# Performance work log

Hardware: AMD Instinct MI355X
Metric: run time of the kernel (lower is better)

## Reference

```python
import jax, jax.numpy as jnp
import numpy as np

B, N, IN_C, OUT_C, H, M, E = 1, 20000, 256, 64, 4, 30, 320000
EPS = 1e-6


def _projection_matrix(m, d, seed=0):
    # NodeFormer create_projection_matrix: stacked transposed-QR blocks, rows
    # rescaled by norms of iid gaussian rows (scaling=0).
    rng = np.random.RandomState(seed)
    blocks = []
    nb_full = m // d
    for _ in range(nb_full):
        q, _ = np.linalg.qr(rng.randn(d, d))
        blocks.append(q.T)
    rem = m - nb_full * d
    if rem > 0:
        q, _ = np.linalg.qr(rng.randn(d, d))
        blocks.append(q.T[:rem])
    final = np.vstack(blocks)
    multiplier = np.linalg.norm(rng.randn(m, d), axis=1)
    return jnp.asarray(multiplier[:, None] * final, dtype=jnp.float32)


def _linear(key, out_f, in_f):
    k1, k2 = jax.random.split(key)
    s = 1.0 / np.sqrt(in_f)
    w = jax.random.uniform(k1, (out_f, in_f), jnp.float32, -s, s)
    b = jax.random.uniform(k2, (out_f,), jnp.float32, -s, s)
    return w, b


def setup_inputs() -> dict:
    key = jax.random.key(0)
    ks = jax.random.split(key, 8)
    Wq_w, Wq_b = _linear(ks[3], H * OUT_C, IN_C)
    Wk_w, Wk_b = _linear(ks[4], H * OUT_C, IN_C)
    Wv_w, Wv_b = _linear(ks[5], H * OUT_C, IN_C)
    Wo_w, Wo_b = _linear(ks[6], OUT_C, H * OUT_C)
    return {
        'z': jax.random.normal(ks[0], (B, N, IN_C), jnp.float32),
        'feat': jax.random.normal(ks[1], (B, N, IN_C), jnp.float32),
        'edge_index': jax.random.randint(ks[2], (2, E), 0, N),
        'tau': jnp.asarray(0.25, jnp.float32),
        'Wq_w': Wq_w, 'Wq_b': Wq_b,
        'Wk_w': Wk_w, 'Wk_b': Wk_b,
        'Wv_w': Wv_w, 'Wv_b': Wv_b,
        'Wo_w': Wo_w, 'Wo_b': Wo_b,
        'b_param': jnp.full((1, H), 0.1, jnp.float32),  # rb_order=1, sigmoid init
        'proj': _projection_matrix(M, OUT_C),
    }


def _softmax_kernel(x, proj, is_query):
    # Performer positive softmax kernel feature map. x: [B,N,H,D] -> [B,N,H,M]
    d = x.shape[-1]
    x = x * (float(d) ** -0.25)
    ratio = 1.0 / jnp.sqrt(jnp.asarray(proj.shape[0], x.dtype))
    xd = jnp.einsum('bnhd,md->bnhm', x, proj)
    diag = 0.5 * jnp.sum(x * x, axis=-1, keepdims=True)
    if is_query:
        mx = jnp.max(xd, axis=-1, keepdims=True)
    else:
        mx = jnp.max(jnp.max(xd, axis=-1, keepdims=True), axis=1, keepdims=True)
    return ratio * (jnp.exp(xd - diag - mx) + EPS)


def reference(z, feat, edge_index, tau, Wq_w, Wq_b, Wk_w, Wk_b, Wv_w, Wv_b,
              Wo_w, Wo_b, b_param, proj):
    Bn, Nn = z.shape[0], z.shape[1]
    q = (feat @ Wq_w.T + Wq_b).reshape(Bn, Nn, H, OUT_C)
    k = (feat @ Wk_w.T + Wk_b).reshape(Bn, Nn, H, OUT_C)
    v = (z @ Wv_w.T + Wv_b).reshape(Bn, Nn, H, OUT_C)

    inv = 1.0 / jnp.sqrt(tau)
    qp = _softmax_kernel(q * inv, proj, True)    # [B,N,H,M]
    kp = _softmax_kernel(k * inv, proj, False)   # [B,N,H,M]

    # Linear (kernelized) attention, O(N*H*M*D)
    kvs = jnp.einsum('bnhm,bnhd->bhmd', kp, v)
    num = jnp.einsum('bnhm,bhmd->bnhd', qp, kvs)
    den = jnp.einsum('bnhm,bhm->bnh', qp, jnp.sum(kp, axis=1))[..., None]
    z_next = num / den                            # [B,N,H,D]

    # Relational bias: GCN-style normalized scatter with per-head scalar weight
    row, col = edge_index[0], edge_index[1]
    d_in = jnp.zeros((Nn,), z.dtype).at[col].add(1.0)
    d_out = jnp.zeros((Nn,), z.dtype).at[row].add(1.0)
    edge_w = jnp.nan_to_num(jnp.sqrt(1.0 / d_in[col]) * jnp.sqrt(1.0 / d_out[row]),
                            nan=0.0, posinf=0.0, neginf=0.0)    # [E]
    msgs = v[:, row] * edge_w[None, :, None, None]              # [B,E,H,D]
    agg = jnp.zeros_like(v).at[:, col].add(msgs)                # [B,N,H,D]
    z_next = z_next + jax.nn.sigmoid(b_param[0])[None, None, :, None] * agg

    out = z_next.reshape(Bn, Nn, H * OUT_C) @ Wo_w.T + Wo_b     # [B,N,OUT_C]
    return out
```

## Files before the change

### kernel.cpp

```cpp
#include <hip/hip_runtime.h>

#define NN 20000
#define EE 320000
#define RATIO_F 0.18257418583505536f
#define EPS_F 1e-6f
#define SCALE_D4 0.35355339059327373f
#define NCH 157

typedef _Float16 f16x8 __attribute__((ext_vector_type(8)));
typedef _Float16 f16x4 __attribute__((ext_vector_type(4)));
typedef float f32x4 __attribute__((ext_vector_type(4)));

__device__ __forceinline__ unsigned fenc(float x) {
  unsigned u = __float_as_uint(x);
  return (u & 0x80000000u) ? ~u : (u | 0x80000000u);
}
__device__ __forceinline__ float fdec(unsigned u) {
  return (u & 0x80000000u) ? __uint_as_float(u & 0x7FFFFFFFu) : __uint_as_float(~u);
}
__device__ __forceinline__ void fma4(float* a, float s, float4 b) {
  a[0] = fmaf(s, b.x, a[0]);
  a[1] = fmaf(s, b.y, a[1]);
  a[2] = fmaf(s, b.z, a[2]);
  a[3] = fmaf(s, b.w, a[3]);
}
__device__ __forceinline__ void gload16(const void* g, void* l) {
  __builtin_amdgcn_global_load_lds(
      (const __attribute__((address_space(1))) unsigned int*)g,
      (__attribute__((address_space(3))) unsigned int*)l, 16, 0, 0);
}

__global__ __launch_bounds__(256)
void k0_build(const float* __restrict__ Wq, const float* __restrict__ Wk,
              const float* __restrict__ Wv, const float* __restrict__ bq,
              const float* __restrict__ bk, const float* __restrict__ bv,
              const float* __restrict__ proj, const float* __restrict__ tau,
              _Float16* __restrict__ Wf, float* __restrict__ bbig) {
  const int col = blockIdx.x;
  const int i = threadIdx.x;
  const float s = rsqrtf(tau[0]) * SCALE_D4;
  float val = 0.f, bias = 0.f;
  if (col < 256) {
    val = Wq[col * 256 + i]; bias = bq[col];
  } else if (col < 512) {
    const int c = col - 256;
    val = Wk[c * 256 + i]; bias = bk[c];
  } else if (col < 768) {
    const int c = col - 512;
    val = Wv[c * 256 + i]; bias = bv[c];
  } else {
    const int rr = col - 768;
    const int grp = rr >> 7;
    const int h = (rr >> 5) & 3, m = rr & 31;
    if (m < 30) {
      const float* W = grp ? Wk : Wq;
      const float* bb = grp ? bk : bq;
      float a = 0.f, ba = 0.f;
#pragma unroll 8
      for (int d = 0; d < 64; ++d) {
        const float pr = proj[m * 64 + d];
        a  = fmaf(pr, W[(h * 64 + d) * 256 + i], a);
        ba = fmaf(pr, bb[h * 64 + d], ba);
      }
      val = s * a; bias = s * ba;
    }
  }
  const int kt = i >> 5, gg = (i >> 3) & 3, j = i & 7;
  const int lane = gg * 16 + (col & 15);
  const size_t off = (size_t)((col >> 4) * 8 + kt) * 512 + lane * 8 + j;
  Wf[off] = (_Float16)val;
  if (i == 0) bbig[col] = bias;
}

__global__ __launch_bounds__(256)
void k0b_wo(const float* __restrict__ Wo, _Float16* __restrict__ WoFh,
            _Float16* __restrict__ WoFl) {
  const int col = blockIdx.x;
  const int i = threadIdx.x;
  const float val = Wo[col * 256 + i];
  const int kt = i >> 5, gg = (i >> 3) & 3, j = i & 7;
  const int lane = gg * 16 + (col & 15);
  const size_t off = (size_t)((col >> 4) * 8 + kt) * 512 + lane * 8 + j;
  const _Float16 hb = (_Float16)val;
  WoFh[off] = hb;
  WoFl[off] = (_Float16)(val - (float)hb);
}

__device__ __forceinline__ void cvt_half(const float4* raw, f16x8* Ah, f16x8* Al) {
#pragma unroll
  for (int kt = 0; kt < 4; ++kt) {
    const float ff[8] = {raw[kt*2].x, raw[kt*2].y, raw[kt*2].z, raw[kt*2].w,
                         raw[kt*2+1].x, raw[kt*2+1].y, raw[kt*2+1].z, raw[kt*2+1].w};
    union { _Float16 h[8]; f16x8 v; } hu, lu;
#pragma unroll
    for (int j = 0; j < 8; ++j) {
      const _Float16 hb = (_Float16)ff[j];
      hu.h[j] = hb;
      lu.h[j] = (_Float16)(ff[j] - (float)hb);
    }
    Ah[kt] = hu.v; Al[kt] = lu.v;
  }
}

__device__ __forceinline__ int ct_of(int s, int isv, int h, int y) {
  if (isv) return 32 + (y - 4) * 8 + s;
  if (s < 4)  return h * 4 + s;
  if (s < 8)  return 16 + h * 4 + (s - 4);
  if (s < 10) return 48 + 2 * h + (s - 8);
  return 56 + 2 * h + (s - 10);
}

__global__ __launch_bounds__(512, 4)
void k1_all(const float* __restrict__ feat, const float* __restrict__ zin,
            const _Float16* __restrict__ Wf, const float* __restrict__ bbig,
            const float* __restrict__ tau,
            float* __restrict__ qp, float* __restrict__ kbuf,
            _Float16* __restrict__ vh, unsigned* __restrict__ kmaxU) {
  __shared__ __align__(16) _Float16 blds[12 * 2048];
  const int t = threadIdx.x;
  const int wid = t >> 6, lane = t & 63;
  const int g = lane >> 4, cl = lane & 15;
  const int y = blockIdx.y;
  const int h = y & 3;
  const int rbase = blockIdx.x * 128 + wid * 16;
  int arow = rbase + cl; if (arow > NN - 1) arow = NN - 1;

  if (y < 4) {
    const float* arp = feat + (size_t)arow * 256;
#pragma unroll
    for (int r = 0; r < 6; ++r) {
      const int idx = r * 4096 + t * 8;
      const int s = idx >> 11, wi = idx & 2047;
      gload16(Wf + (size_t)ct_of(s, 0, h, y) * 4096 + wi, &blds[idx]);
    }
    float4 raw[8];
#pragma unroll
    for (int l = 0; l < 4; ++l) {
      raw[l * 2]     = *(const float4*)(arp + l * 32 + g * 8);
      raw[l * 2 + 1] = *(const float4*)(arp + l * 32 + g * 8 + 4);
    }
    f16x8 Ah[4], Al[4];
    cvt_half(raw, Ah, Al);
    __syncthreads();
#pragma unroll
    for (int l = 0; l < 4; ++l) {
      raw[l * 2]     = *(const float4*)(arp + (l + 4) * 32 + g * 8);
      raw[l * 2 + 1] = *(const float4*)(arp + (l + 4) * 32 + g * 8 + 4);
    }
    f32x4 acc[12];
#pragma unroll
    for (int s = 0; s < 12; ++s) acc[s] = (f32x4){0.f, 0.f, 0.f, 0.f};
#pragma unroll
    for (int ktl = 0; ktl < 4; ++ktl) {
#pragma unroll
      for (int s = 0; s < 12; ++s) {
        const f16x8 b = *(const f16x8*)&blds[s * 2048 + ktl * 512 + lane * 8];
        acc[s] = __builtin_amdgcn_mfma_f32_16x16x32_f16(Ah[ktl], b, acc[s], 0, 0, 0);
        acc[s] = __builtin_amdgcn_mfma_f32_16x16x32_f16(Al[ktl], b, acc[s], 0, 0, 0);
      }
    }
    __syncthreads();
#pragma unroll
    for (int r = 0; r < 6; ++r) {
      const int idx = r * 4096 + t * 8;
      const int s = idx >> 11, wi = idx & 2047;
      gload16(Wf + (size_t)ct_of(s, 0, h, y) * 4096 + 2048 + wi, &blds[idx]);
    }
    cvt_half(raw, Ah, Al);
    __syncthreads();
#pragma unroll
    for (int ktl = 0; ktl < 4; ++ktl) {
#pragma unroll
      for (int s = 0; s < 12; ++s) {
        const f16x8 b = *(const f16x8*)&blds[s * 2048 + ktl * 512 + lane * 8];
        acc[s] = __builtin_amdgcn_mfma_f32_16x16x32_f16(Ah[ktl], b, acc[s], 0, 0, 0);
        acc[s] = __builtin_amdgcn_mfma_f32_16x16x32_f16(Al[ktl], b, acc[s], 0, 0, 0);
      }
    }
#pragma unroll
    for (int s = 0; s < 12; ++s) {
      const float bb = bbig[ct_of(s, 0, h, y) * 16 + cl];
#pragma unroll
      for (int j = 0; j < 4; ++j) acc[s][j] += bb;
    }
    const float sc = rsqrtf(tau[0]) * SCALE_D4;
    const float h2 = 0.5f * sc * sc;
    float dsq[4], dsk[4];
#pragma unroll
    for (int j = 0; j < 4; ++j) {
      dsq[j] = acc[0][j] * acc[0][j] + acc[1][j] * acc[1][j] +
               acc[2][j] * acc[2][j] + acc[3][j] * acc[3][j];
      dsk[j] = acc[4][j] * acc[4][j] + acc[5][j] * acc[5][j] +
               acc[6][j] * acc[6][j] + acc[7][j] * acc[7][j];
    }
#pragma unroll
    for (int m = 1; m < 16; m <<= 1) {
#pragma unroll
      for (int j = 0; j < 4; ++j) {
        dsq[j] += __shfl_xor(dsq[j], m);
        dsk[j] += __shfl_xor(dsk[j], m);
      }
    }
    {
#pragma unroll
      for (int j = 0; j < 4; ++j) {
        const float x0 = acc[8][j], x1 = acc[9][j];
        float mv = fmaxf(x0, (cl < 14) ? x1 : -3.4e38f);
#pragma unroll
        for (int m = 1; m < 16; m <<= 1) mv = fmaxf(mv, __shfl_xor(mv, m));
        const float dg = h2 * dsq[j];
        const int r = rbase + 4 * g + j;
        if (r < NN) {
          float* dst = qp + (size_t)r * 120 + h * 30;
          dst[cl] = RATIO_F * (expf(x0 - dg - mv) + EPS_F);
          if (cl < 14) dst[16 + cl] = RATIO_F * (expf(x1 - dg - mv) + EPS_F);
        }
      }
    }
    {
      float wmax = -3.4e38f;
#pragma unroll
      for (int j = 0; j < 4; ++j) {
        const float x0 = acc[10][j], x1 = acc[11][j];
        float mv = fmaxf(x0, (cl < 14) ? x1 : -3.4e38f);
#pragma unroll
        for (int m = 1; m < 16; m <<= 1) mv = fmaxf(mv, __shfl_xor(mv, m));
        wmax = fmaxf(wmax, mv);
        const float dg = h2 * dsk[j];
        const int r = rbase + 4 * g + j;
        if (r < NN) {
          float* dst = kbuf + (size_t)r * 120 + h * 30;
          dst[cl] = x0 - dg;
          if (cl < 14) dst[16 + cl] = x1 - dg;
        }
      }
      wmax = fmaxf(wmax, __shfl_xor(wmax, 16));
      wmax = fmaxf(wmax, __shfl_xor(wmax, 32));
      if (lane == 0) atomicMax(&kmaxU[h], fenc(wmax));
    }
  } else {
    const float* arp = zin + (size_t)arow * 256;
#pragma unroll
    for (int r = 0; r < 4; ++r) {
      const int idx = r * 4096 + t * 8;
      const int s = idx >> 11, wi = idx & 2047;
      gload16(Wf + (size_t)ct_of(s, 1, h, y) * 4096 + wi, &blds[idx]);
    }
    float4 raw[8];
#pragma unroll
    for (int l = 0; l < 4; ++l) {
      raw[l * 2]     = *(const float4*)(arp + l * 32 + g * 8);
      raw[l * 2 + 1] = *(const float4*)(arp + l * 32 + g * 8 + 4);
    }
    f16x8 Ah[4], Al[4];
    cvt_half(raw, Ah, Al);
    __syncthreads();
#pragma unroll
    for (int l = 0; l < 4; ++l) {
      raw[l * 2]     = *(const float4*)(arp + (l + 4) * 32 + g * 8);
      raw[l * 2 + 1] = *(const float4*)(arp + (l + 4) * 32 + g * 8 + 4);
    }
    f32x4 acc[8];
#pragma unroll
    for (int s = 0; s < 8; ++s) acc[s] = (f32x4){0.f, 0.f, 0.f, 0.f};
#pragma unroll
    for (int ktl = 0; ktl < 4; ++ktl) {
#pragma unroll
      for (int s = 0; s < 8; ++s) {
        const f16x8 b = *(const f16x8*)&blds[s * 2048 + ktl * 512 + lane * 8];
        acc[s] = __builtin_amdgcn_mfma_f32_16x16x32_f16(Ah[ktl], b, acc[s], 0, 0, 0);
        acc[s] = __builtin_amdgcn_mfma_f32_16x16x32_f16(Al[ktl], b, acc[s], 0, 0, 0);
      }
    }
    __syncthreads();
#pragma unroll
    for (int r = 0; r < 4; ++r) {
      const int idx = r * 4096 + t * 8;
      const int s = idx >> 11, wi = idx & 2047;
      gload16(Wf + (size_t)ct_of(s, 1, h, y) * 4096 + 2048 + wi, &blds[idx]);
    }
    cvt_half(raw, Ah, Al);
    __syncthreads();
#pragma unroll
    for (int ktl = 0; ktl < 4; ++ktl) {
#pragma unroll
      for (int s = 0; s < 8; ++s) {
        const f16x8 b = *(const f16x8*)&blds[s * 2048 + ktl * 512 + lane * 8];
        acc[s] = __builtin_amdgcn_mfma_f32_16x16x32_f16(Ah[ktl], b, acc[s], 0, 0, 0);
        acc[s] = __builtin_amdgcn_mfma_f32_16x16x32_f16(Al[ktl], b, acc[s], 0, 0, 0);
      }
    }
#pragma unroll
    for (int s = 0; s < 8; ++s) {
      const int ct = ct_of(s, 1, h, y);
      const float bb = bbig[ct * 16 + cl];
      const int colb = (ct - 32) * 16 + cl;
#pragma unroll
      for (int j = 0; j < 4; ++j) {
        const int r = rbase + 4 * g + j;
        if (r < NN) vh[(size_t)r * 256 + colb] = (_Float16)(acc[s][j] + bb);
      }
    }
  }
}

__global__ __launch_bounds__(256)
void k3_kvs(const float* __restrict__ kbr, const _Float16* __restrict__ vh,
            const unsigned* __restrict__ kmaxU, float* __restrict__ partial) {
  __shared__ float kpch[128 * 32];
  __shared__ float vch[128 * 68];
  const int h = blockIdx.y;
  const int n0 = blockIdx.x * 128;
  const int cnt = min(128, NN - n0);
  const int t = threadIdx.x;
  const float mx = fdec(kmaxU[h]);
  const int m = t >> 3, dg = t & 7, d0 = dg * 8;
#pragma unroll
  for (int l = 0; l < 15; ++l) {
    const int flat = l * 256 + t;
    const int nl = flat / 30, mm = flat - nl * 30;
    kpch[nl * 32 + mm] = (nl < cnt)
        ? RATIO_F * (expf(kbr[(size_t)(n0 + nl) * 120 + h * 30 + mm] - mx) + EPS_F)
        : 0.f;
  }
#pragma unroll
  for (int l = 0; l < 8; ++l) {
    const int f4 = l * 256 + t;
    const int nl = f4 >> 4, dd = (f4 & 15) * 4;
    float4 vv = make_float4(0.f, 0.f, 0.f, 0.f);
    if (nl < cnt) {
      f16x4 u = *(const f16x4*)(vh + (size_t)(n0 + nl) * 256 + h * 64 + dd);
      vv = make_float4((float)u[0], (float)u[1], (float)u[2], (float)u[3]);
    }
    *(float4*)&vch[nl * 68 + dd] = vv;
  }
  __syncthreads();
  float acc[8] = {0, 0, 0, 0, 0, 0, 0, 0};
  float asum = 0.f;
  const int ms = (m < 30) ? m : 0;
  for (int nl = 0; nl < cnt; ++nl) {
    const float kv = kpch[nl * 32 + ms];
    const float4 va = *(const float4*)&vch[nl * 68 + d0];
    const float4 vb = *(const float4*)&vch[nl * 68 + d0 + 4];
    fma4(&acc[0], kv, va);
    fma4(&acc[4], kv, vb);
    asum += kv;
  }
  if (m < 30) {
    float* dst = partial + ((size_t)blockIdx.y * NCH + blockIdx.x) * 1952 + m * 64 + d0;
#pragma unroll
    for (int j = 0; j < 8; ++j) dst[j] = acc[j];
    if (dg == 0)
      partial[((size_t)blockIdx.y * NCH + blockIdx.x) * 1952 + 1920 + m] = asum;
  }
}

__global__ __launch_bounds__(256)
void k3b_reduce(const float* __restrict__ partial, float* __restrict__ kvs,
                float* __restrict__ ksum) {
  const int idx = blockIdx.x * 256 + threadIdx.x;
  if (idx >= 4 * 1952) return;
  const int h = idx / 1952, q = idx - h * 1952;
  float s = 0.f;
  for (int c = 0; c < NCH; ++c)
    s += partial[((size_t)h * NCH + c) * 1952 + q];
  if (q < 1920) kvs[h * 1920 + q] = s;
  else if (q < 1950) ksum[h * 30 + (q - 1920)] = s;
}

__global__ __launch_bounds__(256)
void k4_attn(const float* __restrict__ qp, const float* __restrict__ kvs,
             const float* __restrict__ ksum, float* __restrict__ zbuf) {
  __shared__ float kvsl[120 * 68];
  __shared__ float ksl[120];
  __shared__ float qpl[32 * 120];
  const int t = threadIdx.x;
  const int n0 = blockIdx.x * 32;
#pragma unroll
  for (int l = 0; l < 30; ++l) {
    const int f = l * 256 + t;
    const int hm = f >> 6, d = f & 63;
    kvsl[hm * 68 + d] = kvs[f];
  }
  if (t < 120) ksl[t] = ksum[t];
#pragma unroll
  for (int l = 0; l < 15; ++l) {
    const int f = l * 256 + t;
    qpl[f] = qp[(size_t)n0 * 120 + f];
  }
  __syncthreads();
  const int nl = t >> 3, dg = t & 7, d0 = dg * 8;
  const float* qrow = &qpl[nl * 120];
  float den[4] = {0, 0, 0, 0};
  for (int m = 0; m < 30; ++m) {
#pragma unroll
    for (int hh = 0; hh < 4; ++hh) den[hh] = fmaf(qrow[hh * 30 + m], ksl[hh * 30 + m], den[hh]);
  }
  float acc[4][8] = {};
  for (int m = 0; m < 30; ++m) {
#pragma unroll
    for (int hh = 0; hh < 4; ++hh) {
      const float qv = qrow[hh * 30 + m];
      const float* kr = &kvsl[(hh * 30 + m) * 68 + d0];
      const float4 ka = *(const float4*)kr;
      const float4 kb = *(const float4*)(kr + 4);
      fma4(&acc[hh][0], qv, ka);
      fma4(&acc[hh][4], qv, kb);
    }
  }
  const size_t n = n0 + nl;
#pragma unroll
  for (int hh = 0; hh < 4; ++hh) {
    const float inv = 1.0f / den[hh];
    float4 o1 = make_float4(acc[hh][0] * inv, acc[hh][1] * inv, acc[hh][2] * inv, acc[hh][3] * inv);
    float4 o2 = make_float4(acc[hh][4] * inv, acc[hh][5] * inv, acc[hh][6] * inv, acc[hh][7] * inv);
    *(float4*)(zbuf + n * 256 + hh * 64 + d0) = o1;
    *(float4*)(zbuf + n * 256 + hh * 64 + d0 + 4) = o2;
  }
}

__global__ __launch_bounds__(256)
void k5_deg(const int* __restrict__ ei, int* __restrict__ dini, int* __restrict__ douti) {
  const int q = blockIdx.x * 256 + threadIdx.x;
  if (q >= EE / 4) return;
  const int4 r4 = *(const int4*)(ei + q * 4);
  const int4 c4 = *(const int4*)(ei + EE + q * 4);
  atomicAdd(&dini[c4.x], 1); atomicAdd(&dini[c4.y], 1);
  atomicAdd(&dini[c4.z], 1); atomicAdd(&dini[c4.w], 1);
  atomicAdd(&douti[r4.x], 1); atomicAdd(&douti[r4.y], 1);
  atomicAdd(&douti[r4.z], 1); atomicAdd(&douti[r4.w], 1);
}

__global__ __launch_bounds__(1024)
void k6a_scan(const int* __restrict__ cnt, int* __restrict__ off) {
  __shared__ int s[1024];
  const int t = threadIdx.x;
  int4 v[5];
  int sum = 0;
  const int4* p4 = (const int4*)(cnt + t * 20);
#pragma unroll
  for (int i = 0; i < 5; ++i) {
    v[i] = p4[i];
    sum += v[i].x + v[i].y + v[i].z + v[i].w;
  }
  s[t] = sum;
  __syncthreads();
  for (int o = 1; o < 1024; o <<= 1) {
    const int add = (t >= o) ? s[t - o] : 0;
    __syncthreads();
    s[t] += add;
    __syncthreads();
  }
  int run = (t == 0) ? 0 : s[t - 1];
  if (t == 0) off[0] = 0;
  const int base = t * 20;
#pragma unroll
  for (int i = 0; i < 5; ++i) {
    const int vals[4] = {v[i].x, v[i].y, v[i].z, v[i].w};
#pragma unroll
    for (int j = 0; j < 4; ++j) {
      const int idx = base + i * 4 + j;
      if (idx < NN) { run += vals[j]; off[idx + 1] = run; }
    }
  }
}

__global__ __launch_bounds__(256)
void k6b_fill(const int* __restrict__ ei, const int* __restrict__ coff,
              int* __restrict__ cursor, int* __restrict__ crow) {
  const int e = blockIdx.x * 256 + threadIdx.x;
  const int r = ei[e], c = ei[EE + e];
  const int pos = atomicAdd(&cursor[c], 1);
  crow[coff[c] + pos] = r;
}

__global__ __launch_bounds__(256)
void k6c_rw(const int* __restrict__ douti, float* __restrict__ rw) {
  const int n = blockIdx.x * 256 + threadIdx.x;
  if (n < NN) rw[n] = rsqrtf((float)douti[n]);
}

__global__ __launch_bounds__(256)
void k7g_gather(const int* __restrict__ coff, const int* __restrict__ crow,
                const float* __restrict__ rw, const _Float16* __restrict__ vh,
                _Float16* __restrict__ aggh) {
  const int node = blockIdx.x * 4 + (threadIdx.x >> 6);
  const int lane = threadIdx.x & 63;
  const int o0 = coff[node], o1 = coff[node + 1];
  float a0 = 0.f, a1 = 0.f, a2 = 0.f, a3 = 0.f;
  if (o1 > o0) {
    int e = o0;
    for (; e + 8 <= o1; e += 8) {
      int rr[8];
#pragma unroll
      for (int u = 0; u < 8; ++u) rr[u] = crow[e + u];
      float ww[8];
#pragma unroll
      for (int u = 0; u < 8; ++u) ww[u] = rw[rr[u]];
#pragma unroll
      for (int u = 0; u < 8; ++u) {
        const f16x4 vv = *(const f16x4*)(vh + (size_t)rr[u] * 256 + lane * 4);
        a0 = fmaf(ww[u], (float)vv[0], a0);
        a1 = fmaf(ww[u], (float)vv[1], a1);
        a2 = fmaf(ww[u], (float)vv[2], a2);
        a3 = fmaf(ww[u], (float)vv[3], a3);
      }
    }
    for (; e < o1; ++e) {
      const int r = crow[e];
      const float wr = rw[r];
      const f16x4 vv = *(const f16x4*)(vh + (size_t)r * 256 + lane * 4);
      a0 = fmaf(wr, (float)vv[0], a0);
      a1 = fmaf(wr, (float)vv[1], a1);
      a2 = fmaf(wr, (float)vv[2], a2);
      a3 = fmaf(wr, (float)vv[3], a3);
    }
    const float rin = rsqrtf((float)(o1 - o0));
    a0 *= rin; a1 *= rin; a2 *= rin; a3 *= rin;
  }
  f16x4 st;
  st[0] = (_Float16)a0; st[1] = (_Float16)a1;
  st[2] = (_Float16)a2; st[3] = (_Float16)a3;
  *(f16x4*)(aggh + (size_t)node * 256 + lane * 4) = st;
}

__global__ __launch_bounds__(512, 4)
void k8m_out(const float* __restrict__ zbuf, const _Float16* __restrict__ aggh,
             const _Float16* __restrict__ WoFh, const _Float16* __restrict__ WoFl,
             const float* __restrict__ bo, const float* __restrict__ bp,
             float* __restrict__ out) {
  __shared__ __align__(16) _Float16 blds[8 * 4096];
  const int t = threadIdx.x;
  const int wid = t >> 6, lane = t & 63;
  const int g = lane >> 4, cl = lane & 15;
  const int rbase = blockIdx.x * 128 + wid * 16;
  int arow = rbase + cl; if (arow > NN - 1) arow = NN - 1;
#pragma unroll
  for (int s = 0; s < 4; ++s) {
    gload16(WoFh + (size_t)s * 4096 + t * 8, &blds[(s * 512 + t) * 8]);
    gload16(WoFl + (size_t)s * 4096 + t * 8, &blds[((s + 4) * 512 + t) * 8]);
  }
  float sgv[4];
#pragma unroll
  for (int hh = 0; hh < 4; ++hh) sgv[hh] = 1.f / (1.f + expf(-bp[hh]));
  const float* zr = zbuf + (size_t)arow * 256;
  const _Float16* ar = aggh + (size_t)arow * 256;
  f16x8 Ah[8], Al[8];
#pragma unroll
  for (int kt = 0; kt < 8; ++kt) {
    const float4 z0 = *(const float4*)(zr + kt * 32 + g * 8);
    const float4 z1 = *(const float4*)(zr + kt * 32 + g * 8 + 4);
    const f16x4 g0 = *(const f16x4*)(ar + kt * 32 + g * 8);
    const f16x4 g1 = *(const f16x4*)(ar + kt * 32 + g * 8 + 4);
    const float sg = sgv[kt >> 1];
    const float ff[8] = {
        z0.x + sg * (float)g0[0], z0.y + sg * (float)g0[1],
        z0.z + sg * (float)g0[2], z0.w + sg * (float)g0[3],
        z1.x + sg * (float)g1[0], z1.y + sg * (float)g1[1],
        z1.z + sg * (float)g1[2], z1.w + sg * (float)g1[3]};
    union { _Float16 h[8]; f16x8 v; } hu, lu;
#pragma unroll
    for (int j = 0; j < 8; ++j) {
      const _Float16 hb = (_Float16)ff[j];
      hu.h[j] = hb;
      lu.h[j] = (_Float16)(ff[j] - (float)hb);
    }
    Ah[kt] = hu.v; Al[kt] = lu.v;
  }
  __syncthreads();
  f32x4 acc[4];
#pragma unroll
  for (int s = 0; s < 4; ++s) acc[s] = (f32x4){0.f, 0.f, 0.f, 0.f};
#pragma unroll
  for (int kt = 0; kt < 8; ++kt) {
#pragma unroll
    for (int s = 0; s < 4; ++s) {
      const f16x8 bh = *(const f16x8*)&blds[s * 4096 + kt * 512 + lane * 8];
      const f16x8 bl = *(const f16x8*)&blds[(s + 4) * 4096 + kt * 512 + lane * 8];
      acc[s] = __builtin_amdgcn_mfma_f32_16x16x32_f16(Ah[kt], bh, acc[s], 0, 0, 0);
      acc[s] = __builtin_amdgcn_mfma_f32_16x16x32_f16(Ah[kt], bl, acc[s], 0, 0, 0);
      acc[s] = __builtin_amdgcn_mfma_f32_16x16x32_f16(Al[kt], bh, acc[s], 0, 0, 0);
    }
  }
#pragma unroll
  for (int s = 0; s < 4; ++s) {
    const float bb = bo[s * 16 + cl];
#pragma unroll
    for (int j = 0; j < 4; ++j) {
      const int r = rbase + 4 * g + j;
      if (r < NN) out[(size_t)r * 64 + s * 16 + cl] = acc[s][j] + bb;
    }
  }
}

extern "C" void kernel_launch(void* const* d_in, const int* in_sizes, int n_in,
                              void* d_out, int out_size, void* d_ws, size_t ws_size,
                              hipStream_t stream) {
  (void)in_sizes; (void)n_in; (void)out_size; (void)ws_size;
  const float* z    = (const float*)d_in[0];
  const float* feat = (const float*)d_in[1];
  const int*   ei   = (const int*)d_in[2];
  const float* tau  = (const float*)d_in[3];
  const float* Wq_w = (const float*)d_in[4];
  const float* Wq_b = (const float*)d_in[5];
  const float* Wk_w = (const float*)d_in[6];
  const float* Wk_b = (const float*)d_in[7];
  const float* Wv_w = (const float*)d_in[8];
  const float* Wv_b = (const float*)d_in[9];
  const float* Wo_w = (const float*)d_in[10];
  const float* Wo_b = (const float*)d_in[11];
  const float* bp   = (const float*)d_in[12];
  const float* proj = (const float*)d_in[13];
  float* out = (float*)d_out;

  char* p = (char*)d_ws;
  auto alloc = [&](size_t bytes) { char* r = p; p += (bytes + 255) & ~(size_t)255; return r; };
  _Float16* Wf    = (_Float16*)alloc((size_t)256 * 1024 * 2);
  _Float16* WoFh  = (_Float16*)alloc((size_t)64 * 256 * 2);
  _Float16* WoFl  = (_Float16*)alloc((size_t)64 * 256 * 2);
  float*    bbig  = (float*)alloc(1024 * 4);
  _Float16* vh    = (_Float16*)alloc((size_t)NN * 256 * 2);
  _Float16* aggh  = (_Float16*)alloc((size_t)NN * 256 * 2);
  float*    qp    = (float*)alloc((size_t)NN * 120 * 4);
  float*    kbuf  = (float*)alloc((size_t)NN * 120 * 4);
  float*    zbuf  = (float*)alloc((size_t)NN * 256 * 4);
  float*    partial = (float*)alloc((size_t)4 * NCH * 1952 * 4);
  float*    kvs   = (float*)alloc(7680 * 4);
  float*    ksum  = (float*)alloc(120 * 4);
  float*    rw    = (float*)alloc((size_t)NN * 4);
  char* z0 = p;
  unsigned* kmaxU = (unsigned*)alloc(16);
  int*      dini  = (int*)alloc((size_t)20480 * 4);
  int*      douti = (int*)alloc((size_t)NN * 4);
  int*      cursor= (int*)alloc((size_t)NN * 4);
  char* z1 = p;
  int*      coff  = (int*)alloc((size_t)(NN + 1) * 4);
  int*      crow  = (int*)alloc((size_t)EE * 4);

  hipMemsetAsync(z0, 0, (size_t)(z1 - z0), stream);

  k0_build<<<1024, 256, 0, stream>>>(Wq_w, Wk_w, Wv_w, Wq_b, Wk_b, Wv_b, proj, tau, Wf, bbig);
  k0b_wo<<<64, 256, 0, stream>>>(Wo_w, WoFh, WoFl);
  k5_deg<<<(EE / 4 + 255) / 256, 256, 0, stream>>>(ei, dini, douti);
  k6a_scan<<<1, 1024, 0, stream>>>(dini, coff);
  k6b_fill<<<EE / 256, 256, 0, stream>>>(ei, coff, cursor, crow);
  k6c_rw<<<(NN + 255) / 256, 256, 0, stream>>>(douti, rw);
  k1_all<<<dim3(157, 6), 512, 0, stream>>>(feat, z, Wf, bbig, tau, qp, kbuf, vh, kmaxU);
  k7g_gather<<<NN / 4, 256, 0, stream>>>(coff, crow, rw, vh, aggh);
  k3_kvs<<<dim3(NCH, 4), 256, 0, stream>>>(kbuf, vh, kmaxU, partial);
  k3b_reduce<<<(4 * 1952 + 255) / 256, 256, 0, stream>>>(partial, kvs, ksum);
  k4_attn<<<NN / 32, 256, 0, stream>>>(qp, kvs, ksum, zbuf);
  k8m_out<<<157, 512, 0, stream>>>(zbuf, aggh, WoFh, WoFl, Wo_b, bp, out);
}
```

Baseline: 280.5 us.

## Store qp and z in fp16, fuse bias-add into attention, merge small kernels

The query feature map qp and the pre-output activation z are now stored as fp16 instead of fp32, which halves their memory traffic. The sigmoid-weighted relational-bias add moves from the output GEMM into k4_attn. The output GEMM drops the low-part split MFMA for activations, so it runs two MFMAs per tile instead of three. The Wo conversion kernel merges into k0_build and the fill and rw kernels merge into one launch, cutting launch overhead. The cost is reduced precision in the activations feeding the final projection.

Result: faster. 257.2 us (-8.3%).

```diff
diff --git a/kernel.cpp b/kernel.cpp
--- a/kernel.cpp
+++ b/kernel.cpp
@@ -35,9 +35,23 @@
               const float* __restrict__ Wv, const float* __restrict__ bq,
               const float* __restrict__ bk, const float* __restrict__ bv,
               const float* __restrict__ proj, const float* __restrict__ tau,
-              _Float16* __restrict__ Wf, float* __restrict__ bbig) {
-  const int col = blockIdx.x;
+              const float* __restrict__ Wo,
+              _Float16* __restrict__ Wf, float* __restrict__ bbig,
+              _Float16* __restrict__ WoFh, _Float16* __restrict__ WoFl) {
+  const int blk = blockIdx.x;
   const int i = threadIdx.x;
+  const int kt = i >> 5, gg = (i >> 3) & 3, j = i & 7;
+  if (blk >= 1024) {
+    const int col = blk - 1024;
+    const float val = Wo[col * 256 + i];
+    const int lane = gg * 16 + (col & 15);
+    const size_t off = (size_t)((col >> 4) * 8 + kt) * 512 + lane * 8 + j;
+    const _Float16 hb = (_Float16)val;
+    WoFh[off] = hb;
+    WoFl[off] = (_Float16)(val - (float)hb);
+    return;
+  }
+  const int col = blk;
   const float s = rsqrtf(tau[0]) * SCALE_D4;
   float val = 0.f, bias = 0.f;
   if (col < 256) {
@@ -65,25 +79,10 @@
       val = s * a; bias = s * ba;
     }
   }
-  const int kt = i >> 5, gg = (i >> 3) & 3, j = i & 7;
   const int lane = gg * 16 + (col & 15);
   const size_t off = (size_t)((col >> 4) * 8 + kt) * 512 + lane * 8 + j;
   Wf[off] = (_Float16)val;
   if (i == 0) bbig[col] = bias;
-}
-
-__global__ __launch_bounds__(256)
-void k0b_wo(const float* __restrict__ Wo, _Float16* __restrict__ WoFh,
-            _Float16* __restrict__ WoFl) {
-  const int col = blockIdx.x;
-  const int i = threadIdx.x;
-  const float val = Wo[col * 256 + i];
-  const int kt = i >> 5, gg = (i >> 3) & 3, j = i & 7;
-  const int lane = gg * 16 + (col & 15);
-  const size_t off = (size_t)((col >> 4) * 8 + kt) * 512 + lane * 8 + j;
-  const _Float16 hb = (_Float16)val;
-  WoFh[off] = hb;
-  WoFl[off] = (_Float16)(val - (float)hb);
 }
 
 __device__ __forceinline__ void cvt_half(const float4* raw, f16x8* Ah, f16x8* Al) {
@@ -114,7 +113,7 @@
 void k1_all(const float* __restrict__ feat, const float* __restrict__ zin,
             const _Float16* __restrict__ Wf, const float* __restrict__ bbig,
             const float* __restrict__ tau,
-            float* __restrict__ qp, float* __restrict__ kbuf,
+            _Float16* __restrict__ qph, float* __restrict__ kbuf,
             _Float16* __restrict__ vh, unsigned* __restrict__ kmaxU) {
   __shared__ __align__(16) _Float16 blds[12 * 2048];
   const int t = threadIdx.x;
@@ -211,9 +210,10 @@
         const float dg = h2 * dsq[j];
         const int r = rbase + 4 * g + j;
         if (r < NN) {
-          float* dst = qp + (size_t)r * 120 + h * 30;
-          dst[cl] = RATIO_F * (expf(x0 - dg - mv) + EPS_F);
-          if (cl < 14) dst[16 + cl] = RATIO_F * (expf(x1 - dg - mv) + EPS_F);
+          _Float16* dst = qph + (size_t)r * 120 + h * 30;
+          dst[cl] = (_Float16)(RATIO_F * (expf(x0 - dg - mv) + EPS_F));
+          if (cl < 14)
+            dst[16 + cl] = (_Float16)(RATIO_F * (expf(x1 - dg - mv) + EPS_F));
         }
       }
     }
@@ -369,8 +369,9 @@
 }
 
 __global__ __launch_bounds__(256)
-void k4_attn(const float* __restrict__ qp, const float* __restrict__ kvs,
-             const float* __restrict__ ksum, float* __restrict__ zbuf) {
+void k4_attn(const _Float16* __restrict__ qph, const float* __restrict__ kvs,
+             const float* __restrict__ ksum, const _Float16* __restrict__ aggh,
+             const float* __restrict__ bp, _Float16* __restrict__ zh) {
   __shared__ float kvsl[120 * 68];
   __shared__ float ksl[120];
   __shared__ float qpl[32 * 120];
@@ -386,7 +387,7 @@
 #pragma unroll
   for (int l = 0; l < 15; ++l) {
     const int f = l * 256 + t;
-    qpl[f] = qp[(size_t)n0 * 120 + f];
+    qpl[f] = (float)qph[(size_t)n0 * 120 + f];
   }
   __syncthreads();
   const int nl = t >> 3, dg = t & 7, d0 = dg * 8;
@@ -412,10 +413,13 @@
 #pragma unroll
   for (int hh = 0; hh < 4; ++hh) {
     const float inv = 1.0f / den[hh];
-    float4 o1 = make_float4(acc[hh][0] * inv, acc[hh][1] * inv, acc[hh][2] * inv, acc[hh][3] * inv);
-    float4 o2 = make_float4(acc[hh][4] * inv, acc[hh][5] * inv, acc[hh][6] * inv, acc[hh][7] * inv);
-    *(float4*)(zbuf + n * 256 + hh * 64 + d0) = o1;
-    *(float4*)(zbuf + n * 256 + hh * 64 + d0 + 4) = o2;
+    const float sg = 1.f / (1.f + expf(-bp[hh]));
+    const f16x8 ag = *(const f16x8*)(aggh + n * 256 + hh * 64 + d0);
+    f16x8 o;
+#pragma unroll
+    for (int jj = 0; jj < 8; ++jj)
+      o[jj] = (_Float16)(acc[hh][jj] * inv + sg * (float)ag[jj]);
+    *(f16x8*)(zh + n * 256 + hh * 64 + d0) = o;
   }
 }
 
@@ -466,18 +470,19 @@
 }
 
 __global__ __launch_bounds__(256)
-void k6b_fill(const int* __restrict__ ei, const int* __restrict__ coff,
-              int* __restrict__ cursor, int* __restrict__ crow) {
-  const int e = blockIdx.x * 256 + threadIdx.x;
-  const int r = ei[e], c = ei[EE + e];
-  const int pos = atomicAdd(&cursor[c], 1);
-  crow[coff[c] + pos] = r;
-}
-
-__global__ __launch_bounds__(256)
-void k6c_rw(const int* __restrict__ douti, float* __restrict__ rw) {
-  const int n = blockIdx.x * 256 + threadIdx.x;
-  if (n < NN) rw[n] = rsqrtf((float)douti[n]);
+void k6bc(const int* __restrict__ ei, const int* __restrict__ coff,
+          int* __restrict__ cursor, int* __restrict__ crow,
+          const int* __restrict__ douti, float* __restrict__ rw) {
+  const int b = blockIdx.x;
+  if (b < EE / 256) {
+    const int e = b * 256 + threadIdx.x;
+    const int r = ei[e], c = ei[EE + e];
+    const int pos = atomicAdd(&cursor[c], 1);
+    crow[coff[c] + pos] = r;
+  } else {
+    const int n = (b - EE / 256) * 256 + threadIdx.x;
+    if (n < NN) rw[n] = rsqrtf((float)douti[n]);
+  }
 }
 
 __global__ __launch_bounds__(256)
@@ -525,9 +530,8 @@
 }
 
 __global__ __launch_bounds__(512, 4)
-void k8m_out(const float* __restrict__ zbuf, const _Float16* __restrict__ aggh,
-             const _Float16* __restrict__ WoFh, const _Float16* __restrict__ WoFl,
-             const float* __restrict__ bo, const float* __restrict__ bp,
+void k8m_out(const _Float16* __restrict__ zh, const _Float16* __restrict__ WoFh,
+             const _Float16* __restrict__ WoFl, const float* __restrict__ bo,
              float* __restrict__ out) {
   __shared__ __align__(16) _Float16 blds[8 * 4096];
   const int t = threadIdx.x;
@@ -540,33 +544,11 @@
     gload16(WoFh + (size_t)s * 4096 + t * 8, &blds[(s * 512 + t) * 8]);
     gload16(WoFl + (size_t)s * 4096 + t * 8, &blds[((s + 4) * 512 + t) * 8]);
   }
-  float sgv[4];
-#pragma unroll
-  for (int hh = 0; hh < 4; ++hh) sgv[hh] = 1.f / (1.f + expf(-bp[hh]));
-  const float* zr = zbuf + (size_t)arow * 256;
-  const _Float16* ar = aggh + (size_t)arow * 256;
-  f16x8 Ah[8], Al[8];
-#pragma unroll
-  for (int kt = 0; kt < 8; ++kt) {
-    const float4 z0 = *(const float4*)(zr + kt * 32 + g * 8);
-    const float4 z1 = *(const float4*)(zr + kt * 32 + g * 8 + 4);
-    const f16x4 g0 = *(const f16x4*)(ar + kt * 32 + g * 8);
-    const f16x4 g1 = *(const f16x4*)(ar + kt * 32 + g * 8 + 4);
-    const float sg = sgv[kt >> 1];
-    const float ff[8] = {
-        z0.x + sg * (float)g0[0], z0.y + sg * (float)g0[1],
-        z0.z + sg * (float)g0[2], z0.w + sg * (float)g0[3],
-        z1.x + sg * (float)g1[0], z1.y + sg * (float)g1[1],
-        z1.z + sg * (float)g1[2], z1.w + sg * (float)g1[3]};
-    union { _Float16 h[8]; f16x8 v; } hu, lu;
-#pragma unroll
-    for (int j = 0; j < 8; ++j) {
-      const _Float16 hb = (_Float16)ff[j];
-      hu.h[j] = hb;
-      lu.h[j] = (_Float16)(ff[j] - (float)hb);
-    }
-    Ah[kt] = hu.v; Al[kt] = lu.v;
-  }
+  const _Float16* zr = zh + (size_t)arow * 256;
+  f16x8 Ah[8];
+#pragma unroll
+  for (int kt = 0; kt < 8; ++kt)
+    Ah[kt] = *(const f16x8*)(zr + kt * 32 + g * 8);
   __syncthreads();
   f32x4 acc[4];
 #pragma unroll
@@ -579,7 +561,6 @@
       const f16x8 bl = *(const f16x8*)&blds[(s + 4) * 4096 + kt * 512 + lane * 8];
       acc[s] = __builtin_amdgcn_mfma_f32_16x16x32_f16(Ah[kt], bh, acc[s], 0, 0, 0);
       acc[s] = __builtin_amdgcn_mfma_f32_16x16x32_f16(Ah[kt], bl, acc[s], 0, 0, 0);
-      acc[s] = __builtin_amdgcn_mfma_f32_16x16x32_f16(Al[kt], bh, acc[s], 0, 0, 0);
     }
   }
 #pragma unroll
@@ -621,9 +602,9 @@
   float*    bbig  = (float*)alloc(1024 * 4);
   _Float16* vh    = (_Float16*)alloc((size_t)NN * 256 * 2);
   _Float16* aggh  = (_Float16*)alloc((size_t)NN * 256 * 2);
-  float*    qp    = (float*)alloc((size_t)NN * 120 * 4);
+  _Float16* qph   = (_Float16*)alloc((size_t)NN * 120 * 2);
   float*    kbuf  = (float*)alloc((size_t)NN * 120 * 4);
-  float*    zbuf  = (float*)alloc((size_t)NN * 256 * 4);
+  _Float16* zh    = (_Float16*)alloc((size_t)NN * 256 * 2);
   float*    partial = (float*)alloc((size_t)4 * NCH * 1952 * 4);
   float*    kvs   = (float*)alloc(7680 * 4);
   float*    ksum  = (float*)alloc(120 * 4);
@@ -639,16 +620,16 @@
 
   hipMemsetAsync(z0, 0, (size_t)(z1 - z0), stream);
 
-  k0_build<<<1024, 256, 0, stream>>>(Wq_w, Wk_w, Wv_w, Wq_b, Wk_b, Wv_b, proj, tau, Wf, bbig);
-  k0b_wo<<<64, 256, 0, stream>>>(Wo_w, WoFh, WoFl);
+  k0_build<<<1088, 256, 0, stream>>>(Wq_w, Wk_w, Wv_w, Wq_b, Wk_b, Wv_b, proj,
+                                     tau, Wo_w, Wf, bbig, WoFh, WoFl);
   k5_deg<<<(EE / 4 + 255) / 256, 256, 0, stream>>>(ei, dini, douti);
   k6a_scan<<<1, 1024, 0, stream>>>(dini, coff);
-  k6b_fill<<<EE / 256, 256, 0, stream>>>(ei, coff, cursor, crow);
-  k6c_rw<<<(NN + 255) / 256, 256, 0, stream>>>(douti, rw);
-  k1_all<<<dim3(157, 6), 512, 0, stream>>>(feat, z, Wf, bbig, tau, qp, kbuf, vh, kmaxU);
+  k6bc<<<EE / 256 + (NN + 255) / 256, 256, 0, stream>>>(ei, coff, cursor, crow,
+                                                        douti, rw);
+  k1_all<<<dim3(157, 6), 512, 0, stream>>>(feat, z, Wf, bbig, tau, qph, kbuf, vh, kmaxU);
   k7g_gather<<<NN / 4, 256, 0, stream>>>(coff, crow, rw, vh, aggh);
   k3_kvs<<<dim3(NCH, 4), 256, 0, stream>>>(kbuf, vh, kmaxU, partial);
   k3b_reduce<<<(4 * 1952 + 255) / 256, 256, 0, stream>>>(partial, kvs, ksum);
-  k4_attn<<<NN / 32, 256, 0, stream>>>(qp, kvs, ksum, zbuf);
-  k8m_out<<<157, 512, 0, stream>>>(zbuf, aggh, WoFh, WoFl, Wo_b, bp, out);
-}
+  k4_attn<<<NN / 32, 256, 0, stream>>>(qph, kvs, ksum, aggh, bp, zh);
+  k8m_out<<<157, 512, 0, stream>>>(zh, WoFh, WoFl, Wo_b, out);
+}
```
